# Performance work log

Measured on AMD Instinct MI355X. Metric: run time of the kernel, lower is better.

## Reference

```python
import jax, jax.numpy as jnp
import numpy as np

N = 50000   # num_nodes
H = 128     # n_hidden
C = 16      # num_classes
R = 8       # num_rels
B = 4       # num_bases
E = 800000  # num_edges


def setup_inputs() -> dict:
    key = jax.random.key(0)
    ks = jax.random.split(key, 20)
    s = 0.05
    return {
        "src": jax.random.randint(ks[0], (E,), 0, N),
        "dst": jax.random.randint(ks[1], (E,), 0, N),
        "h": jnp.arange(N),                      # node IDs (first layer in_feat == num_nodes)
        "r": jax.random.randint(ks[2], (E,), 0, R),
        "norm": jax.random.uniform(ks[3], (E, 1), dtype=jnp.float32),
        # layer 0: basis weights over [num_nodes -> H]
        "bases0": jax.random.normal(ks[4], (B, N, H), dtype=jnp.float32) * s,
        "wcomp0": jax.random.normal(ks[5], (R, B), dtype=jnp.float32) * s,
        "loop0": jax.random.normal(ks[6], (N, H), dtype=jnp.float32) * s,
        "bias0": jnp.zeros((H,), dtype=jnp.float32),
        # layer 1: H -> H
        "bases1": jax.random.normal(ks[7], (B, H, H), dtype=jnp.float32) * s,
        "wcomp1": jax.random.normal(ks[8], (R, B), dtype=jnp.float32) * s,
        "loop1": jax.random.normal(ks[9], (H, H), dtype=jnp.float32) * s,
        "bias1": jnp.zeros((H,), dtype=jnp.float32),
        # layer 2: H -> C
        "bases2": jax.random.normal(ks[10], (B, H, C), dtype=jnp.float32) * s,
        "wcomp2": jax.random.normal(ks[11], (R, B), dtype=jnp.float32) * s,
        "loop2": jax.random.normal(ks[12], (H, C), dtype=jnp.float32) * s,
        "bias2": jnp.zeros((C,), dtype=jnp.float32),
    }


def _agg(msg, dst):
    return jax.ops.segment_sum(msg, dst, num_segments=N)


def _layer_id(ids, src, dst, r, norm, bases, wcomp, loop, bias):
    # first layer: input features are node IDs -> embedding lookup into composed weight
    w = jnp.einsum('rb,bnf->rnf', wcomp, bases)      # [R, N, H]
    msg = w[r, ids[src]] * norm                      # [E, H] gather per edge
    out = _agg(msg, dst) + loop[ids] + bias          # aggregate + self-loop + bias
    return jax.nn.relu(out)


def _layer_dense(x, src, dst, r, norm, bases, wcomp, loop, bias, act):
    w = jnp.einsum('rb,bdf->rdf', wcomp, bases)      # [R, d_in, d_out]
    trans = jnp.einsum('nd,rdf->rnf', x, w)          # [R, N, d_out] (all rel transforms)
    msg = trans[r, src] * norm                       # [E, d_out] relation-indexed gather
    out = _agg(msg, dst) + x @ loop + bias
    return jax.nn.relu(out) if act else out


def reference(src, dst, h, r, norm,
              bases0, wcomp0, loop0, bias0,
              bases1, wcomp1, loop1, bias1,
              bases2, wcomp2, loop2, bias2):
    x = _layer_id(h, src, dst, r, norm, bases0, wcomp0, loop0, bias0)
    x = _layer_dense(x, src, dst, r, norm, bases1, wcomp1, loop1, bias1, act=True)
    x = _layer_dense(x, src, dst, r, norm, bases2, wcomp2, loop2, bias2, act=False)
    return x
```

## Files before the change

kernel.cpp:

```cpp
#include <hip/hip_runtime.h>

#define NN 50000
#define NP 50048
#define HH 128
#define CC 16
#define RRL 8
#define BB 4
#define EE 800000
#define NT (RRL * NN)
#define SCAN_CHUNK 2048
#define NBLK_SCAN ((NT + SCAN_CHUNK - 1) / SCAN_CHUNK)
#define KBIG 1152
#define W0B_BLOCKS ((NN * 16) / 256)
#define COMPOSE_THREADS (HH * KBIG + RRL * CC * HH + CC * HH)
#define COMPOSE_BLOCKS ((COMPOSE_THREADS + 255) / 256)
#define NC 98
#define CAP 10240
#define SPLIT 2
#define CHUNK_E 4096
#define PA_BLOCKS ((EE + CHUNK_E - 1) / CHUNK_E)

typedef short bf16x8_t __attribute__((ext_vector_type(8)));
typedef float f32x4_t __attribute__((ext_vector_type(4)));
typedef float f32x2_t __attribute__((ext_vector_type(2)));

__device__ __forceinline__ unsigned short f2bf(float f) {
  unsigned int x = __float_as_uint(f);
  unsigned int r = x + 0x7fffu + ((x >> 16) & 1u);
  return (unsigned short)(r >> 16);
}
__device__ __forceinline__ float bflo(unsigned int u) { return __uint_as_float(u << 16); }
__device__ __forceinline__ float bfhi(unsigned int u) {
  return __uint_as_float(u & 0xffff0000u);
}
__device__ __forceinline__ void acc8v(f32x2_t* a, uint4 v, float nrm) {
  f32x2_t nn = {nrm, nrm};
  f32x2_t u0 = {bflo(v.x), bfhi(v.x)};
  f32x2_t u1 = {bflo(v.y), bfhi(v.y)};
  f32x2_t u2 = {bflo(v.z), bfhi(v.z)};
  f32x2_t u3 = {bflo(v.w), bfhi(v.w)};
  a[0] += nn * u0;
  a[1] += nn * u1;
  a[2] += nn * u2;
  a[3] += nn * u3;
}


__global__ __launch_bounds__(256) void scanA_kernel(const int* __restrict__ cnt,
                                                    int* __restrict__ off,
                                                    int* __restrict__ partials) {
  __shared__ int sums[256];
  int tid = threadIdx.x;
  int base = blockIdx.x * SCAN_CHUNK + tid * 8;
  int v[8];
  int s = 0;
#pragma unroll
  for (int j = 0; j < 8; ++j) {
    int idx = base + j;
    v[j] = (idx < NT) ? cnt[idx] : 0;
    s += v[j];
  }
  sums[tid] = s;
  __syncthreads();
  for (int o = 1; o < 256; o <<= 1) {
    int t = (tid >= o) ? sums[tid - o] : 0;
    __syncthreads();
    sums[tid] += t;
    __syncthreads();
  }
  int run = sums[tid] - s;
#pragma unroll
  for (int j = 0; j < 8; ++j) {
    int idx = base + j;
    if (idx < NT) off[idx] = run;
    run += v[j];
  }
  if (tid == 255) partials[blockIdx.x] = sums[255];
}

__global__ __launch_bounds__(256) void scanB_kernel(const int* __restrict__ partials,
                                                    int* __restrict__ pexcl) {
  __shared__ int sums[256];
  int tid = threadIdx.x;
  int p = (tid < NBLK_SCAN) ? partials[tid] : 0;
  sums[tid] = p;
  __syncthreads();
  for (int o = 1; o < 256; o <<= 1) {
    int t = (tid >= o) ? sums[tid - o] : 0;
    __syncthreads();
    sums[tid] += t;
    __syncthreads();
  }
  if (tid < NBLK_SCAN) pexcl[tid] = sums[tid] - p;
}

__global__ __launch_bounds__(256) void addC_kernel(int* __restrict__ off,
                                                   const int* __restrict__ pexcl,
                                                   int* __restrict__ cur) {
  int tid = threadIdx.x;
  int add = pexcl[blockIdx.x];
  int base = blockIdx.x * SCAN_CHUNK + tid * 8;
#pragma unroll
  for (int j = 0; j < 8; ++j) {
    int idx = base + j;
    if (idx < NT) {
      int v = off[idx] + add;
      off[idx] = v;
      cur[idx] = v;
    }
  }
  if (blockIdx.x == 0 && tid == 0) off[NT] = EE;
}


__global__ __launch_bounds__(256) void partitionA_kernel(
    const int* __restrict__ r, const int* __restrict__ dst, const int* __restrict__ src,
    const int* __restrict__ h, const float* __restrict__ norm, int* __restrict__ cnt2,
    int* __restrict__ tmpCur, unsigned* __restrict__ tmpK, uint2* __restrict__ tmpP,
    unsigned* __restrict__ tmpW) {
  __shared__ int hist[NC];
  __shared__ int run[NC];
  int tid = threadIdx.x;
  int base = blockIdx.x * CHUNK_E;
  for (int i = tid; i < NC; i += 256) hist[i] = 0;
  __syncthreads();
#pragma unroll
  for (int j = 0; j < CHUNK_E / 256; ++j) {
    int e = base + tid + j * 256;
    if (e < EE) atomicAdd(&hist[dst[e] >> 9], 1);
  }
  __syncthreads();
  if (tid < NC && hist[tid] > 0)
    run[tid] = tid * CAP + atomicAdd(&tmpCur[tid], hist[tid]);
  __syncthreads();
#pragma unroll
  for (int j = 0; j < CHUNK_E / 256; ++j) {
    int e = base + tid + j * 256;
    if (e < EE) {
      int d = dst[e], z = r[e];
      int key = d * RRL + z;
      atomicAdd(&cnt2[key], 1);
      int c = d >> 9;
      int pos = atomicAdd(&run[c], 1);
      int sv = src[e];
      tmpK[pos] = (unsigned)key;
      uint2 pay;
      pay.x = (unsigned)sv | ((unsigned)z << 24);
      pay.y = __float_as_uint(norm[e]);
      tmpP[pos] = pay;
      tmpW[pos] = (unsigned)h[sv] * 8u + (unsigned)z;
    }
  }
}


__global__ __launch_bounds__(256) void placeB_kernel(const int* __restrict__ tmpCur,
                                                     const unsigned* __restrict__ tmpK,
                                                     const uint2* __restrict__ tmpP,
                                                     const unsigned* __restrict__ tmpW,
                                                     int* __restrict__ cur2,
                                                     uint2* __restrict__ ep1,
                                                     uint2* __restrict__ epw) {
  int c = blockIdx.x / SPLIT, q = blockIdx.x % SPLIT;
  int cnt = tmpCur[c];
  int qb = (cnt * q) / SPLIT;
  int qe = (cnt * (q + 1)) / SPLIT;
  int base = c * CAP;
  for (int i = qb + threadIdx.x; i < qe; i += 256) {
    unsigned key = tmpK[base + i];
    uint2 pay = tmpP[base + i];
    unsigned w = tmpW[base + i];
    int pos = atomicAdd(&cur2[key], 1);
    ep1[pos] = pay;
    epw[pos] = (uint2){w, pay.y};
  }
}


__global__ __launch_bounds__(256) void prep_weights_kernel(
    const float* __restrict__ bases0, const float* __restrict__ wcomp0,
    unsigned short* __restrict__ w0b, const float* __restrict__ wcomp1,
    const float* __restrict__ bases1, const float* __restrict__ loop1,
    const float* __restrict__ wcomp2, const float* __restrict__ bases2,
    const float* __restrict__ loop2, unsigned short* __restrict__ w1big,
    unsigned short* __restrict__ w2t, unsigned short* __restrict__ loop2t) {
  if (blockIdx.x < W0B_BLOCKS) {
    int idx = blockIdx.x * 256 + threadIdx.x;
    int m = idx >> 4, c8 = idx & 15;
    float4 a[BB][2];
#pragma unroll
    for (int b = 0; b < BB; ++b) {
      const float4* sp = (const float4*)(bases0 + ((size_t)b * NN + m) * HH + c8 * 8);
      a[b][0] = sp[0];
      a[b][1] = sp[1];
    }
    uint4* orow = (uint4*)w0b + (size_t)m * 128 + c8;
#pragma unroll
    for (int z = 0; z < RRL; ++z) {
      float c0 = wcomp0[z * BB + 0], c1 = wcomp0[z * BB + 1];
      float c2 = wcomp0[z * BB + 2], c3 = wcomp0[z * BB + 3];
      float e[8];
#pragma unroll
      for (int q = 0; q < 2; ++q) {
        e[q * 4 + 0] = c0 * a[0][q].x + c1 * a[1][q].x + c2 * a[2][q].x + c3 * a[3][q].x;
        e[q * 4 + 1] = c0 * a[0][q].y + c1 * a[1][q].y + c2 * a[2][q].y + c3 * a[3][q].y;
        e[q * 4 + 2] = c0 * a[0][q].z + c1 * a[1][q].z + c2 * a[2][q].z + c3 * a[3][q].z;
        e[q * 4 + 3] = c0 * a[0][q].w + c1 * a[1][q].w + c2 * a[2][q].w + c3 * a[3][q].w;
      }
      uint4 pk;
      pk.x = ((unsigned)f2bf(e[1]) << 16) | f2bf(e[0]);
      pk.y = ((unsigned)f2bf(e[3]) << 16) | f2bf(e[2]);
      pk.z = ((unsigned)f2bf(e[5]) << 16) | f2bf(e[4]);
      pk.w = ((unsigned)f2bf(e[7]) << 16) | f2bf(e[6]);
      orow[z * 16] = pk;
    }
    return;
  }
  int idx = (blockIdx.x - W0B_BLOCKS) * 256 + threadIdx.x;
  if (idx < HH * KBIG) {
    int n = idx / KBIG, k = idx - n * KBIG;
    float a;
    if (k < 1024) {
      int z = k >> 7, kk = k & 127;
      a = 0.f;
#pragma unroll
      for (int b = 0; b < BB; ++b)
        a += wcomp1[z * BB + b] * bases1[((size_t)b * HH + kk) * HH + n];
    } else {
      int kk = k - 1024;
      a = loop1[kk * HH + n];
    }
    w1big[idx] = f2bf(a);
    return;
  }
  int j = idx - HH * KBIG;
  if (j < RRL * CC * HH) {
    int z = j >> 11;
    int rem = j & 2047;
    int n = rem >> 7, k = rem & 127;
    float a = 0.f;
#pragma unroll
    for (int b = 0; b < BB; ++b)
      a += wcomp2[z * BB + b] * bases2[((size_t)b * HH + k) * CC + n];
    w2t[j] = f2bf(a);
    return;
  }
  j -= RRL * CC * HH;
  if (j < CC * HH) {
    int n = j >> 7, k = j & 127;
    loop2t[j] = f2bf(loop2[k * CC + n]);
  }
}


__global__ __launch_bounds__(256) void l0_seg_kernel(
    const int* __restrict__ h, const int* __restrict__ off2, const uint2* __restrict__ epw,
    const unsigned short* __restrict__ w0b, const float* __restrict__ loop0,
    const float* __restrict__ bias0, unsigned short* __restrict__ x1b) {
  int lane = threadIdx.x & 63;
  int n = blockIdx.x * 4 + (threadIdx.x >> 6);
  if (n >= NP) return;
  const int g = lane >> 4;
  const int t = lane & 15;
  f32x2_t acc[4];
#pragma unroll
  for (int j = 0; j < 4; ++j) acc[j] = (f32x2_t){0.f, 0.f};

  if (n < NN) {
    int beg = off2[n * RRL];
    int end = off2[n * RRL + RRL];
    int i = beg + g;
    uint2 p0 = {0u, 0u}, p1 = {0u, 0u};
    if (i < end) p0 = epw[i];
    if (i + 4 < end) p1 = epw[i + 4];
    while (i < end) {
      uint2 q0 = {0u, 0u}, q1 = {0u, 0u};
      if (i + 8 < end) q0 = epw[i + 8];
      if (i + 12 < end) q1 = epw[i + 12];
      uint4 va = *(const uint4*)(w0b + (size_t)p0.x * HH + t * 8);
      uint4 vb = *(const uint4*)(w0b + (size_t)p1.x * HH + t * 8);
      acc8v(acc, va, __uint_as_float(p0.y));
      acc8v(acc, vb, __uint_as_float(p1.y));
      i += 8;
      p0 = q0;
      p1 = q1;
    }
  }
  float* af = (float*)acc;
#pragma unroll
  for (int j = 0; j < 8; ++j) {
    af[j] += __shfl_xor(af[j], 16, 64);
    af[j] += __shfl_xor(af[j], 32, 64);
  }
  if (g != 0) return;
  uint4 o = {0u, 0u, 0u, 0u};
  if (n < NN) {
    int hn = h[n];
    float4 l0v = ((const float4*)(loop0 + (size_t)hn * HH))[t * 2];
    float4 l1v = ((const float4*)(loop0 + (size_t)hn * HH))[t * 2 + 1];
    float4 b0v = ((const float4*)bias0)[t * 2];
    float4 b1v = ((const float4*)bias0)[t * 2 + 1];
    float e0 = fmaxf(af[0] + l0v.x + b0v.x, 0.f);
    float e1 = fmaxf(af[1] + l0v.y + b0v.y, 0.f);
    float e2 = fmaxf(af[2] + l0v.z + b0v.z, 0.f);
    float e3 = fmaxf(af[3] + l0v.w + b0v.w, 0.f);
    float e4 = fmaxf(af[4] + l1v.x + b1v.x, 0.f);
    float e5 = fmaxf(af[5] + l1v.y + b1v.y, 0.f);
    float e6 = fmaxf(af[6] + l1v.z + b1v.z, 0.f);
    float e7 = fmaxf(af[7] + l1v.w + b1v.w, 0.f);
    o.x = ((unsigned)f2bf(e1) << 16) | f2bf(e0);
    o.y = ((unsigned)f2bf(e3) << 16) | f2bf(e2);
    o.z = ((unsigned)f2bf(e5) << 16) | f2bf(e4);
    o.w = ((unsigned)f2bf(e7) << 16) | f2bf(e6);
  }
  *(uint4*)(x1b + (size_t)n * HH + t * 8) = o;
}


__global__ __launch_bounds__(256) void l1_agg_kernel(const int* __restrict__ off2,
                                                     const uint2* __restrict__ ep1,
                                                     const unsigned short* __restrict__ x1b,
                                                     unsigned short* __restrict__ AGG) {
  int tid = threadIdx.x;
  int gid = blockIdx.x * 16 + (tid >> 4);
  int l = tid & 15;
  int n = gid >> 3, z = gid & 7;
  if (n >= NP) return;
  unsigned short* orow = AGG + (size_t)n * 1024 + z * 128 + l * 8;
  if (n >= NN) {
    *(uint4*)orow = (uint4){0u, 0u, 0u, 0u};
    return;
  }
  int beg = off2[gid];
  int end = off2[gid + 1];
  f32x2_t a[4];
#pragma unroll
  for (int j = 0; j < 4; ++j) a[j] = (f32x2_t){0.f, 0.f};

  int i = beg;
  uint2 p0 = {0u, 0u}, p1 = {0u, 0u};
  if (i < end) p0 = ep1[i];
  if (i + 1 < end) p1 = ep1[i + 1];
  while (i < end) {
    uint2 q0 = {0u, 0u}, q1 = {0u, 0u};
    if (i + 2 < end) q0 = ep1[i + 2];
    if (i + 3 < end) q1 = ep1[i + 3];
    unsigned s0 = p0.x & 0xFFFFFFu, s1 = p1.x & 0xFFFFFFu;
    uint4 v0 = *(const uint4*)(x1b + (size_t)s0 * HH + l * 8);
    uint4 v1 = *(const uint4*)(x1b + (size_t)s1 * HH + l * 8);
    acc8v(a, v0, __uint_as_float(p0.y));
    acc8v(a, v1, __uint_as_float(p1.y));
    i += 2;
    p0 = q0;
    p1 = q1;
  }
  float* af = (float*)a;
  uint4 o;
  o.x = ((unsigned)f2bf(af[1]) << 16) | f2bf(af[0]);
  o.y = ((unsigned)f2bf(af[3]) << 16) | f2bf(af[2]);
  o.z = ((unsigned)f2bf(af[5]) << 16) | f2bf(af[4]);
  o.w = ((unsigned)f2bf(af[7]) << 16) | f2bf(af[6]);
  *(uint4*)orow = o;
}


__global__ __launch_bounds__(256) void gemm_k1152_kernel(
    const unsigned short* __restrict__ AGG, const unsigned short* __restrict__ x1b,
    const unsigned short* __restrict__ w1big, const float* __restrict__ bias1,
    unsigned short* __restrict__ x2b) {
  constexpr int LP = 136;
  __shared__ unsigned short Alds[64 * LP];
  __shared__ unsigned short Blds[128 * LP];
  const int row0 = blockIdx.x * 64;
  const int tid = threadIdx.x;
  const int w = tid >> 6, lane = tid & 63;
  const int quad = lane >> 4, l15 = lane & 15;
  const int rb = (w >> 1) * 32;
  const int cb = (w & 1) * 64;

  f32x4_t acc[2][4];
#pragma unroll
  for (int rt = 0; rt < 2; ++rt)
#pragma unroll
    for (int ct = 0; ct < 4; ++ct) acc[rt][ct] = (f32x4_t){0.f, 0.f, 0.f, 0.f};

  for (int kb = 0; kb < 9; ++kb) {
    if (kb) __syncthreads();
#pragma unroll
    for (int it = 0; it < 4; ++it) {
      int flat = tid + it * 256;
      int row = flat >> 4, c8 = flat & 15;
      const unsigned short* srcp =
          (kb < 8) ? AGG + (size_t)(row0 + row) * 1024 + kb * 128 + c8 * 8
                   : x1b + (size_t)(row0 + row) * 128 + c8 * 8;
      *(uint4*)(&Alds[row * LP + c8 * 8]) = *(const uint4*)srcp;
    }
#pragma unroll
    for (int it = 0; it < 8; ++it) {
      int flat = tid + it * 256;
      int row = flat >> 4, c8 = flat & 15;
      *(uint4*)(&Blds[row * LP + c8 * 8]) =
          *(const uint4*)(w1big + (size_t)row * KBIG + kb * 128 + c8 * 8);
    }
    __syncthreads();
#pragma unroll
    for (int ks = 0; ks < 4; ++ks) {
      int ko = ks * 32 + quad * 8;
      bf16x8_t af[2], bfr[4];
#pragma unroll
      for (int rt = 0; rt < 2; ++rt)
        af[rt] = *(const bf16x8_t*)(&Alds[(rb + rt * 16 + l15) * LP + ko]);
#pragma unroll
      for (int ct = 0; ct < 4; ++ct)
        bfr[ct] = *(const bf16x8_t*)(&Blds[(cb + ct * 16 + l15) * LP + ko]);
#pragma unroll
      for (int rt = 0; rt < 2; ++rt)
#pragma unroll
        for (int ct = 0; ct < 4; ++ct)
          acc[rt][ct] =
              __builtin_amdgcn_mfma_f32_16x16x32_bf16(af[rt], bfr[ct], acc[rt][ct], 0, 0, 0);
    }
  }
#pragma unroll
  for (int rt = 0; rt < 2; ++rt)
#pragma unroll
    for (int ct = 0; ct < 4; ++ct) {
      int n = cb + ct * 16 + l15;
      float bv = bias1[n];
#pragma unroll
      for (int i = 0; i < 4; ++i) {
        int m = row0 + rb + rt * 16 + quad * 4 + i;
        float val = (m < NN) ? fmaxf(acc[rt][ct][i] + bv, 0.f) : 0.f;
        x2b[(size_t)m * HH + n] = f2bf(val);
      }
    }
}


__global__ __launch_bounds__(256) void l2_trans_kernel(
    const unsigned short* __restrict__ x2b, const unsigned short* __restrict__ w2t,
    const unsigned short* __restrict__ loop2t, const float* __restrict__ bias2,
    unsigned short* __restrict__ trans2, float* __restrict__ out) {
  constexpr int LP = 136;
  __shared__ unsigned short Alds[128 * LP];
  __shared__ unsigned short Blds[9][16 * LP];
  const int row0 = blockIdx.x * 128;
  const int tid = threadIdx.x;

#pragma unroll
  for (int it = 0; it < 8; ++it) {
    int flat = tid + it * 256;
    int row = flat >> 4, c8 = flat & 15;
    *(uint4*)(&Alds[row * LP + c8 * 8]) =
        *(const uint4*)(x2b + ((size_t)(row0 + row)) * 128 + c8 * 8);
  }
  {
    int row = tid >> 4, c8 = tid & 15;
#pragma unroll
    for (int z = 0; z < 9; ++z) {
      const unsigned short* B = (z < 8) ? w2t + (size_t)z * CC * HH : loop2t;
      *(uint4*)(&Blds[z][row * LP + c8 * 8]) = *(const uint4*)(B + row * 128 + c8 * 8);
    }
  }
  __syncthreads();

  const int w = tid >> 6, lane = tid & 63;
  const int quad = lane >> 4, l15 = lane & 15;
  const int rb = w * 32;

  for (int z = 0; z < 9; ++z) {
    f32x4_t acc[2];
    acc[0] = (f32x4_t){0.f, 0.f, 0.f, 0.f};
    acc[1] = (f32x4_t){0.f, 0.f, 0.f, 0.f};
#pragma unroll
    for (int ks = 0; ks < 4; ++ks) {
      int ko = ks * 32 + quad * 8;
      bf16x8_t af0 = *(const bf16x8_t*)(&Alds[(rb + l15) * LP + ko]);
      bf16x8_t af1 = *(const bf16x8_t*)(&Alds[(rb + 16 + l15) * LP + ko]);
      bf16x8_t bfr = *(const bf16x8_t*)(&Blds[z][l15 * LP + ko]);
      acc[0] = __builtin_amdgcn_mfma_f32_16x16x32_bf16(af0, bfr, acc[0], 0, 0, 0);
      acc[1] = __builtin_amdgcn_mfma_f32_16x16x32_bf16(af1, bfr, acc[1], 0, 0, 0);
    }
    if (z < 8) {
      unsigned short* ob = trans2 + (size_t)z * NP * CC;
#pragma unroll
      for (int rt = 0; rt < 2; ++rt)
#pragma unroll
        for (int i = 0; i < 4; ++i) {
          int m = row0 + rb + rt * 16 + quad * 4 + i;
          ob[(size_t)m * CC + l15] = f2bf(acc[rt][i]);
        }
    } else {
      float bv = bias2[l15];
#pragma unroll
      for (int rt = 0; rt < 2; ++rt)
#pragma unroll
        for (int i = 0; i < 4; ++i) {
          int m = row0 + rb + rt * 16 + quad * 4 + i;
          if (m < NN) out[(size_t)m * CC + l15] = acc[rt][i] + bv;
        }
    }
  }
}


__global__ __launch_bounds__(256) void l2_seg_kernel(const int* __restrict__ off2,
                                                     const uint2* __restrict__ ep1,
                                                     const unsigned short* __restrict__ trans2,
                                                     float* __restrict__ outp) {
  int lane = threadIdx.x & 63;
  int n = blockIdx.x * 4 + (threadIdx.x >> 6);
  if (n >= NN) return;
  const int g = lane >> 3;
  const int t = lane & 7;
  float a0 = 0.f, a1 = 0.f;
  int beg = off2[n * RRL];
  int end = off2[n * RRL + RRL];
  int i = beg + g;
  uint2 p0 = {0u, 0u}, p1 = {0u, 0u};
  if (i < end) p0 = ep1[i];
  if (i + 8 < end) p1 = ep1[i + 8];
  while (i < end) {
    uint2 q0 = {0u, 0u}, q1 = {0u, 0u};
    if (i + 16 < end) q0 = ep1[i + 16];
    if (i + 24 < end) q1 = ep1[i + 24];
    unsigned s0 = p0.x & 0xFFFFFFu, z0 = p0.x >> 24;
    unsigned s1 = p1.x & 0xFFFFFFu, z1 = p1.x >> 24;
    unsigned int u0 =
        *(const unsigned int*)(trans2 + ((size_t)z0 * NP + s0) * CC + t * 2);
    unsigned int u1 =
        *(const unsigned int*)(trans2 + ((size_t)z1 * NP + s1) * CC + t * 2);
    float na = __uint_as_float(p0.y), nb = __uint_as_float(p1.y);
    a0 = fmaf(na, bflo(u0), a0);
    a1 = fmaf(na, bfhi(u0), a1);
    a0 = fmaf(nb, bflo(u1), a0);
    a1 = fmaf(nb, bfhi(u1), a1);
    i += 16;
    p0 = q0;
    p1 = q1;
  }
  a0 += __shfl_xor(a0, 8, 64);
  a0 += __shfl_xor(a0, 16, 64);
  a0 += __shfl_xor(a0, 32, 64);
  a1 += __shfl_xor(a1, 8, 64);
  a1 += __shfl_xor(a1, 16, 64);
  a1 += __shfl_xor(a1, 32, 64);
  if (g != 0) return;
  float2* o = (float2*)(outp + (size_t)n * CC) + t;
  float2 cv = *o;
  cv.x += a0;
  cv.y += a1;
  *o = cv;
}


extern "C" void kernel_launch(void* const* d_in, const int* in_sizes, int n_in,
                              void* d_out, int out_size, void* d_ws, size_t ws_size,
                              hipStream_t stream) {
  const int* src = (const int*)d_in[0];
  const int* dst = (const int*)d_in[1];
  const int* h = (const int*)d_in[2];
  const int* r = (const int*)d_in[3];
  const float* norm = (const float*)d_in[4];
  const float* bases0 = (const float*)d_in[5];
  const float* wcomp0 = (const float*)d_in[6];
  const float* loop0 = (const float*)d_in[7];
  const float* bias0 = (const float*)d_in[8];
  const float* bases1 = (const float*)d_in[9];
  const float* wcomp1 = (const float*)d_in[10];
  const float* loop1 = (const float*)d_in[11];
  const float* bias1 = (const float*)d_in[12];
  const float* bases2 = (const float*)d_in[13];
  const float* wcomp2 = (const float*)d_in[14];
  const float* loop2 = (const float*)d_in[15];
  const float* bias2 = (const float*)d_in[16];
  float* out = (float*)d_out;

  char* p = (char*)d_ws;
  auto alloc = [&](size_t bytes) {
    char* q = p;
    p += (bytes + 255) & ~(size_t)255;
    return q;
  };
  unsigned short* x1b = (unsigned short*)alloc((size_t)NP * HH * 2);
  unsigned short* x2b = (unsigned short*)alloc((size_t)NP * HH * 2);
  unsigned short* trans2 = (unsigned short*)alloc((size_t)RRL * NP * CC * 2);
  unsigned short* w1big = (unsigned short*)alloc((size_t)HH * KBIG * 2);
  unsigned short* w2t = (unsigned short*)alloc((size_t)RRL * CC * HH * 2);
  unsigned short* loop2t = (unsigned short*)alloc((size_t)CC * HH * 2);
  uint2* ep1 = (uint2*)alloc((size_t)EE * 8);
  uint2* epw = (uint2*)alloc((size_t)EE * 8);
  unsigned* tmpK = (unsigned*)alloc((size_t)NC * CAP * 4);
  uint2* tmpP = (uint2*)alloc((size_t)NC * CAP * 8);
  unsigned* tmpW = (unsigned*)alloc((size_t)NC * CAP * 4);
  int* off2 = (int*)alloc((size_t)(NT + 1) * 4);
  int* cur2 = (int*)alloc((size_t)NT * 4);
  int* cnt2 = (int*)alloc((size_t)(NT + 256) * 4);
  int* tmpCur = cnt2 + NT;
  int* partials = (int*)alloc(1024);
  int* pexcl = (int*)alloc(1024);
  unsigned short* BIG = (unsigned short*)alloc((size_t)RRL * NP * HH * 2);

  hipMemsetAsync(cnt2, 0, (size_t)(NT + 256) * 4, stream);
  partitionA_kernel<<<PA_BLOCKS, 256, 0, stream>>>(r, dst, src, h, norm, cnt2, tmpCur,
                                                   tmpK, tmpP, tmpW);
  scanA_kernel<<<NBLK_SCAN, 256, 0, stream>>>(cnt2, off2, partials);
  scanB_kernel<<<1, 256, 0, stream>>>(partials, pexcl);
  addC_kernel<<<NBLK_SCAN, 256, 0, stream>>>(off2, pexcl, cur2);
  placeB_kernel<<<NC * SPLIT, 256, 0, stream>>>(tmpCur, tmpK, tmpP, tmpW, cur2, ep1, epw);

  prep_weights_kernel<<<W0B_BLOCKS + COMPOSE_BLOCKS, 256, 0, stream>>>(
      bases0, wcomp0, BIG, wcomp1, bases1, loop1, wcomp2, bases2, loop2, w1big, w2t,
      loop2t);

  l0_seg_kernel<<<NP / 4, 256, 0, stream>>>(h, off2, epw, BIG, loop0, bias0, x1b);

  l1_agg_kernel<<<NP * 8 / 16, 256, 0, stream>>>(off2, ep1, x1b, BIG);
  gemm_k1152_kernel<<<NP / 64, 256, 0, stream>>>(BIG, x1b, w1big, bias1, x2b);

  l2_trans_kernel<<<NP / 128, 256, 0, stream>>>(x2b, w2t, loop2t, bias2, trans2, out);
  l2_seg_kernel<<<(NN + 3) / 4, 256, 0, stream>>>(off2, ep1, trans2, out);
}
```

Before: 477.0 us.

## Fuse edge partition and weight-prep kernels into one front kernel

Merges the edge partition pass and the basis-weight composition pass into a single launch with block-range dispatch, so the bandwidth-heavy bases0 composition runs alongside the atomic-heavy partition. Partition chunks are shrunk from 4096 to 1024 edges to get more blocks, and each w0b thread now handles 16 columns instead of 8. This removes one launch and the serialization between the two independent stages. In exchange it adds more global atomics on tmpCur and uses more registers per w0b thread.

```diff
diff --git a/kernel.cpp b/kernel.cpp
--- a/kernel.cpp
+++ b/kernel.cpp
@@ -11,14 +11,15 @@
 #define SCAN_CHUNK 2048
 #define NBLK_SCAN ((NT + SCAN_CHUNK - 1) / SCAN_CHUNK)
 #define KBIG 1152
-#define W0B_BLOCKS ((NN * 16) / 256)
+#define W0B_BLOCKS ((NN * 8 + 255) / 256)
 #define COMPOSE_THREADS (HH * KBIG + RRL * CC * HH + CC * HH)
 #define COMPOSE_BLOCKS ((COMPOSE_THREADS + 255) / 256)
 #define NC 98
 #define CAP 10240
 #define SPLIT 2
-#define CHUNK_E 4096
+#define CHUNK_E 1024
 #define PA_BLOCKS ((EE + CHUNK_E - 1) / CHUNK_E)
+#define FRONT_BLOCKS (PA_BLOCKS + W0B_BLOCKS + COMPOSE_BLOCKS)
 
 typedef short bf16x8_t __attribute__((ext_vector_type(8)));
 typedef float f32x4_t __attribute__((ext_vector_type(4)));
@@ -113,43 +114,127 @@
 }
 
 
-__global__ __launch_bounds__(256) void partitionA_kernel(
+__global__ __launch_bounds__(256) void front_kernel(
     const int* __restrict__ r, const int* __restrict__ dst, const int* __restrict__ src,
     const int* __restrict__ h, const float* __restrict__ norm, int* __restrict__ cnt2,
     int* __restrict__ tmpCur, unsigned* __restrict__ tmpK, uint2* __restrict__ tmpP,
-    unsigned* __restrict__ tmpW) {
+    unsigned* __restrict__ tmpW, const float* __restrict__ bases0,
+    const float* __restrict__ wcomp0, unsigned short* __restrict__ w0b,
+    const float* __restrict__ wcomp1, const float* __restrict__ bases1,
+    const float* __restrict__ loop1, const float* __restrict__ wcomp2,
+    const float* __restrict__ bases2, const float* __restrict__ loop2,
+    unsigned short* __restrict__ w1big, unsigned short* __restrict__ w2t,
+    unsigned short* __restrict__ loop2t) {
   __shared__ int hist[NC];
   __shared__ int run[NC];
   int tid = threadIdx.x;
-  int base = blockIdx.x * CHUNK_E;
-  for (int i = tid; i < NC; i += 256) hist[i] = 0;
-  __syncthreads();
-#pragma unroll
-  for (int j = 0; j < CHUNK_E / 256; ++j) {
-    int e = base + tid + j * 256;
-    if (e < EE) atomicAdd(&hist[dst[e] >> 9], 1);
-  }
-  __syncthreads();
-  if (tid < NC && hist[tid] > 0)
-    run[tid] = tid * CAP + atomicAdd(&tmpCur[tid], hist[tid]);
-  __syncthreads();
-#pragma unroll
-  for (int j = 0; j < CHUNK_E / 256; ++j) {
-    int e = base + tid + j * 256;
-    if (e < EE) {
-      int d = dst[e], z = r[e];
-      int key = d * RRL + z;
-      atomicAdd(&cnt2[key], 1);
-      int c = d >> 9;
-      int pos = atomicAdd(&run[c], 1);
-      int sv = src[e];
-      tmpK[pos] = (unsigned)key;
-      uint2 pay;
-      pay.x = (unsigned)sv | ((unsigned)z << 24);
-      pay.y = __float_as_uint(norm[e]);
-      tmpP[pos] = pay;
-      tmpW[pos] = (unsigned)h[sv] * 8u + (unsigned)z;
-    }
+  if (blockIdx.x < PA_BLOCKS) {
+    int base = blockIdx.x * CHUNK_E;
+    for (int i = tid; i < NC; i += 256) hist[i] = 0;
+    __syncthreads();
+#pragma unroll
+    for (int j = 0; j < CHUNK_E / 256; ++j) {
+      int e = base + tid + j * 256;
+      if (e < EE) atomicAdd(&hist[dst[e] >> 9], 1);
+    }
+    __syncthreads();
+    if (tid < NC && hist[tid] > 0)
+      run[tid] = tid * CAP + atomicAdd(&tmpCur[tid], hist[tid]);
+    __syncthreads();
+#pragma unroll
+    for (int j = 0; j < CHUNK_E / 256; ++j) {
+      int e = base + tid + j * 256;
+      if (e < EE) {
+        int d = dst[e], z = r[e];
+        int key = d * RRL + z;
+        atomicAdd(&cnt2[key], 1);
+        int c = d >> 9;
+        int pos = atomicAdd(&run[c], 1);
+        int sv = src[e];
+        tmpK[pos] = (unsigned)key;
+        uint2 pay;
+        pay.x = (unsigned)sv | ((unsigned)z << 24);
+        pay.y = __float_as_uint(norm[e]);
+        tmpP[pos] = pay;
+        tmpW[pos] = (unsigned)h[sv] * 8u + (unsigned)z;
+      }
+    }
+    return;
+  }
+  int bx = blockIdx.x - PA_BLOCKS;
+  if (bx < W0B_BLOCKS) {
+    int idx = bx * 256 + tid;
+    int m = idx >> 3, c16 = idx & 7;
+    if (m >= NN) return;
+    float4 a[BB][4];
+#pragma unroll
+    for (int b = 0; b < BB; ++b) {
+      const float4* sp = (const float4*)(bases0 + ((size_t)b * NN + m) * HH + c16 * 16);
+      a[b][0] = sp[0];
+      a[b][1] = sp[1];
+      a[b][2] = sp[2];
+      a[b][3] = sp[3];
+    }
+    uint4* orow = (uint4*)w0b + (size_t)m * 128 + c16 * 2;
+#pragma unroll
+    for (int z = 0; z < RRL; ++z) {
+      float c0 = wcomp0[z * BB + 0], c1 = wcomp0[z * BB + 1];
+      float c2 = wcomp0[z * BB + 2], c3 = wcomp0[z * BB + 3];
+      float e[16];
+#pragma unroll
+      for (int q = 0; q < 4; ++q) {
+        e[q * 4 + 0] = c0 * a[0][q].x + c1 * a[1][q].x + c2 * a[2][q].x + c3 * a[3][q].x;
+        e[q * 4 + 1] = c0 * a[0][q].y + c1 * a[1][q].y + c2 * a[2][q].y + c3 * a[3][q].y;
+        e[q * 4 + 2] = c0 * a[0][q].z + c1 * a[1][q].z + c2 * a[2][q].z + c3 * a[3][q].z;
+        e[q * 4 + 3] = c0 * a[0][q].w + c1 * a[1][q].w + c2 * a[2][q].w + c3 * a[3][q].w;
+      }
+      uint4 pk0, pk1;
+      pk0.x = ((unsigned)f2bf(e[1]) << 16) | f2bf(e[0]);
+      pk0.y = ((unsigned)f2bf(e[3]) << 16) | f2bf(e[2]);
+      pk0.z = ((unsigned)f2bf(e[5]) << 16) | f2bf(e[4]);
+      pk0.w = ((unsigned)f2bf(e[7]) << 16) | f2bf(e[6]);
+      pk1.x = ((unsigned)f2bf(e[9]) << 16) | f2bf(e[8]);
+      pk1.y = ((unsigned)f2bf(e[11]) << 16) | f2bf(e[10]);
+      pk1.z = ((unsigned)f2bf(e[13]) << 16) | f2bf(e[12]);
+      pk1.w = ((unsigned)f2bf(e[15]) << 16) | f2bf(e[14]);
+      orow[z * 16] = pk0;
+      orow[z * 16 + 1] = pk1;
+    }
+    return;
+  }
+  int idx = (bx - W0B_BLOCKS) * 256 + tid;
+  if (idx < HH * KBIG) {
+    int n = idx / KBIG, k = idx - n * KBIG;
+    float a;
+    if (k < 1024) {
+      int z = k >> 7, kk = k & 127;
+      a = 0.f;
+#pragma unroll
+      for (int b = 0; b < BB; ++b)
+        a += wcomp1[z * BB + b] * bases1[((size_t)b * HH + kk) * HH + n];
+    } else {
+      int kk = k - 1024;
+      a = loop1[kk * HH + n];
+    }
+    w1big[idx] = f2bf(a);
+    return;
+  }
+  int j = idx - HH * KBIG;
+  if (j < RRL * CC * HH) {
+    int z = j >> 11;
+    int rem = j & 2047;
+    int n = rem >> 7, k = rem & 127;
+    float a = 0.f;
+#pragma unroll
+    for (int b = 0; b < BB; ++b)
+      a += wcomp2[z * BB + b] * bases2[((size_t)b * HH + k) * CC + n];
+    w2t[j] = f2bf(a);
+    return;
+  }
+  j -= RRL * CC * HH;
+  if (j < CC * HH) {
+    int n = j >> 7, k = j & 127;
+    loop2t[j] = f2bf(loop2[k * CC + n]);
   }
 }
 
@@ -173,82 +258,6 @@
     int pos = atomicAdd(&cur2[key], 1);
     ep1[pos] = pay;
     epw[pos] = (uint2){w, pay.y};
-  }
-}
-
-
-__global__ __launch_bounds__(256) void prep_weights_kernel(
-    const float* __restrict__ bases0, const float* __restrict__ wcomp0,
-    unsigned short* __restrict__ w0b, const float* __restrict__ wcomp1,
-    const float* __restrict__ bases1, const float* __restrict__ loop1,
-    const float* __restrict__ wcomp2, const float* __restrict__ bases2,
-    const float* __restrict__ loop2, unsigned short* __restrict__ w1big,
-    unsigned short* __restrict__ w2t, unsigned short* __restrict__ loop2t) {
-  if (blockIdx.x < W0B_BLOCKS) {
-    int idx = blockIdx.x * 256 + threadIdx.x;
-    int m = idx >> 4, c8 = idx & 15;
-    float4 a[BB][2];
-#pragma unroll
-    for (int b = 0; b < BB; ++b) {
-      const float4* sp = (const float4*)(bases0 + ((size_t)b * NN + m) * HH + c8 * 8);
-      a[b][0] = sp[0];
-      a[b][1] = sp[1];
-    }
-    uint4* orow = (uint4*)w0b + (size_t)m * 128 + c8;
-#pragma unroll
-    for (int z = 0; z < RRL; ++z) {
-      float c0 = wcomp0[z * BB + 0], c1 = wcomp0[z * BB + 1];
-      float c2 = wcomp0[z * BB + 2], c3 = wcomp0[z * BB + 3];
-      float e[8];
-#pragma unroll
-      for (int q = 0; q < 2; ++q) {
-        e[q * 4 + 0] = c0 * a[0][q].x + c1 * a[1][q].x + c2 * a[2][q].x + c3 * a[3][q].x;
-        e[q * 4 + 1] = c0 * a[0][q].y + c1 * a[1][q].y + c2 * a[2][q].y + c3 * a[3][q].y;
-        e[q * 4 + 2] = c0 * a[0][q].z + c1 * a[1][q].z + c2 * a[2][q].z + c3 * a[3][q].z;
-        e[q * 4 + 3] = c0 * a[0][q].w + c1 * a[1][q].w + c2 * a[2][q].w + c3 * a[3][q].w;
-      }
-      uint4 pk;
-      pk.x = ((unsigned)f2bf(e[1]) << 16) | f2bf(e[0]);
-      pk.y = ((unsigned)f2bf(e[3]) << 16) | f2bf(e[2]);
-      pk.z = ((unsigned)f2bf(e[5]) << 16) | f2bf(e[4]);
-      pk.w = ((unsigned)f2bf(e[7]) << 16) | f2bf(e[6]);
-      orow[z * 16] = pk;
-    }
-    return;
-  }
-  int idx = (blockIdx.x - W0B_BLOCKS) * 256 + threadIdx.x;
-  if (idx < HH * KBIG) {
-    int n = idx / KBIG, k = idx - n * KBIG;
-    float a;
-    if (k < 1024) {
-      int z = k >> 7, kk = k & 127;
-      a = 0.f;
-#pragma unroll
-      for (int b = 0; b < BB; ++b)
-        a += wcomp1[z * BB + b] * bases1[((size_t)b * HH + kk) * HH + n];
-    } else {
-      int kk = k - 1024;
-      a = loop1[kk * HH + n];
-    }
-    w1big[idx] = f2bf(a);
-    return;
-  }
-  int j = idx - HH * KBIG;
-  if (j < RRL * CC * HH) {
-    int z = j >> 11;
-    int rem = j & 2047;
-    int n = rem >> 7, k = rem & 127;
-    float a = 0.f;
-#pragma unroll
-    for (int b = 0; b < BB; ++b)
-      a += wcomp2[z * BB + b] * bases2[((size_t)b * HH + k) * CC + n];
-    w2t[j] = f2bf(a);
-    return;
-  }
-  j -= RRL * CC * HH;
-  if (j < CC * HH) {
-    int n = j >> 7, k = j & 127;
-    loop2t[j] = f2bf(loop2[k * CC + n]);
   }
 }
 
@@ -602,17 +611,15 @@
   unsigned short* BIG = (unsigned short*)alloc((size_t)RRL * NP * HH * 2);
 
   hipMemsetAsync(cnt2, 0, (size_t)(NT + 256) * 4, stream);
-  partitionA_kernel<<<PA_BLOCKS, 256, 0, stream>>>(r, dst, src, h, norm, cnt2, tmpCur,
-                                                   tmpK, tmpP, tmpW);
+  front_kernel<<<FRONT_BLOCKS, 256, 0, stream>>>(
+      r, dst, src, h, norm, cnt2, tmpCur, tmpK, tmpP, tmpW, bases0, wcomp0, BIG, wcomp1,
+      bases1, loop1, wcomp2, bases2, loop2, w1big, w2t, loop2t);
+
   scanA_kernel<<<NBLK_SCAN, 256, 0, stream>>>(cnt2, off2, partials);
   scanB_kernel<<<1, 256, 0, stream>>>(partials, pexcl);
   addC_kernel<<<NBLK_SCAN, 256, 0, stream>>>(off2, pexcl, cur2);
   placeB_kernel<<<NC * SPLIT, 256, 0, stream>>>(tmpCur, tmpK, tmpP, tmpW, cur2, ep1, epw);
 
-  prep_weights_kernel<<<W0B_BLOCKS + COMPOSE_BLOCKS, 256, 0, stream>>>(
-      bases0, wcomp0, BIG, wcomp1, bases1, loop1, wcomp2, bases2, loop2, w1big, w2t,
-      loop2t);
-
   l0_seg_kernel<<<NP / 4, 256, 0, stream>>>(h, off2, epw, BIG, loop0, bias0, x1b);
 
   l1_agg_kernel<<<NP * 8 / 16, 256, 0, stream>>>(off2, ep1, x1b, BIG);
```

Measured after the change: 472.9 us. No clear change (-0.9%).
